# Performance work log

Hardware: AMD Instinct MI355X
Metric: run time of the kernel (lower is better)

## Reference

```python
import jax, jax.numpy as jnp
import numpy as np

D_MODEL = 768
N_HEADS = 12
D_K = D_MODEL // N_HEADS
NEG_INF = -1e9


def setup_inputs() -> dict:
    key = jax.random.key(0)
    ks = jax.random.split(key, 7)
    B, S = 4, 2048
    x = jax.random.normal(ks[0], (B, S, D_MODEL), dtype=jnp.float32)
    # causal mask, broadcastable to [B, H, S, S]
    mask = jnp.tril(jnp.ones((S, S), dtype=bool))[None, None, :, :]
    scale = 1.0 / np.sqrt(D_MODEL)
    Wq = jax.random.normal(ks[1], (D_MODEL, D_MODEL), dtype=jnp.float32) * scale
    bq = jnp.zeros((D_MODEL,), dtype=jnp.float32)
    Wk = jax.random.normal(ks[2], (D_MODEL, D_MODEL), dtype=jnp.float32) * scale
    bk = jnp.zeros((D_MODEL,), dtype=jnp.float32)
    Wv = jax.random.normal(ks[3], (D_MODEL, D_MODEL), dtype=jnp.float32) * scale
    bv = jnp.zeros((D_MODEL,), dtype=jnp.float32)
    return {"x": x, "mask": mask, "Wq": Wq, "bq": bq, "Wk": Wk, "bk": bk, "Wv": Wv, "bv": bv}


def reference(x, mask, Wq, bq, Wk, bk, Wv, bv):
    B, S, _ = x.shape
    # projections (torch Linear: y = x @ W.T + b)
    q = (x @ Wq.T + bq).reshape(B, S, N_HEADS, D_K)
    k = (x @ Wk.T + bk).reshape(B, S, N_HEADS, D_K)
    v = (x @ Wv.T + bv).reshape(B, S, N_HEADS, D_K)
    # scores: [B, H, S, S]
    scores = jnp.einsum("bqhd,bkhd->bhqk", q, k) / jnp.sqrt(jnp.float32(D_K))
    scores = jnp.where(mask, scores, NEG_INF)
    probs = jax.nn.softmax(scores, axis=-1)
    # attention: [B, H, S, D_K] -> [B, S, d_model]
    attn = jnp.einsum("bhqk,bkhd->bqhd", probs, v).reshape(B, S, D_MODEL)
    return attn
```

## Files before the change

### kernel.cpp

```cpp
#include <hip/hip_runtime.h>
#include <math.h>


#define S_LEN 2048
#define BATCH 4
#define HEADS 12
#define DM 768
#define DK 64
#define BH (BATCH*HEADS)
#define MROWS (BATCH*S_LEN)
#define QSCALE 0.1803368801111244f

typedef __attribute__((ext_vector_type(8))) short short8;
typedef __attribute__((ext_vector_type(4))) float floatx4;
typedef __attribute__((address_space(3))) unsigned char lds_byte;
typedef __attribute__((address_space(1))) const unsigned char glob_byte;

__device__ __forceinline__ unsigned short f2bf(float f) {
  union { float f; unsigned int u; } a; a.f = f;
  unsigned int u = a.u;
  return (unsigned short)((u + 0x7fffu + ((u >> 16) & 1u)) >> 16);
}
__device__ __forceinline__ unsigned short f2bf_rtz(float f) {
  union { float f; unsigned int u; } a; a.f = f;
  return (unsigned short)(a.u >> 16);
}

__global__ void cast_f32_bf16(const float* __restrict__ src,
                              unsigned short* __restrict__ dst, int n) {
  int i = (blockIdx.x * blockDim.x + threadIdx.x) * 4;
  if (i < n) {
    float4 v = *(const float4*)(src + i);
    ushort4 o;
    o.x = f2bf(v.x); o.y = f2bf(v.y); o.z = f2bf(v.z); o.w = f2bf(v.w);
    *(ushort4*)(dst + i) = o;
  }
}

__global__ void cast_w3(const float* __restrict__ w0, const float* __restrict__ w1,
                        const float* __restrict__ w2, unsigned short* __restrict__ dst,
                        int n) {
  const float* src = (blockIdx.y == 0) ? w0 : (blockIdx.y == 1) ? w1 : w2;
  int i = (blockIdx.x * blockDim.x + threadIdx.x) * 4;
  if (i < n) {
    float4 v = *(const float4*)(src + i);
    ushort4 o;
    o.x = f2bf(v.x); o.y = f2bf(v.y); o.z = f2bf(v.z); o.w = f2bf(v.w);
    *(ushort4*)(dst + (size_t)blockIdx.y * n + i) = o;
  }
}

__global__ __launch_bounds__(256) void qkv_gemm(
    const unsigned short* __restrict__ xb,
    const unsigned short* __restrict__ wb,
    const float* __restrict__ bq, const float* __restrict__ bk,
    const float* __restrict__ bv,
    unsigned short* __restrict__ qo,
    unsigned short* __restrict__ ko,
    unsigned short* __restrict__ vto) {
  __shared__ unsigned short a_lds[128 * 32];
  __shared__ unsigned short b_lds[128 * 32];
  const int mat = blockIdx.z;
  const int tid = threadIdx.x;
  const int wave = tid >> 6, lane = tid & 63, quad = lane >> 4, ln = lane & 15;
  const int wm = wave & 1, wn = wave >> 1;
  const int m_blk = blockIdx.x * 128, n_blk = blockIdx.y * 128;
  const unsigned short* w = wb + (size_t)mat * DM * DM;
  const int srow = lane >> 2, schunk = lane & 3;

  const floatx4 fz = {0.f, 0.f, 0.f, 0.f};
  floatx4 acc[4][4];
#pragma unroll
  for (int mg = 0; mg < 4; mg++)
#pragma unroll
    for (int c = 0; c < 4; c++) acc[mg][c] = fz;

  for (int k0 = 0; k0 < DM; k0 += 32) {
#pragma unroll
    for (int j = 0; j < 2; j++) {
      int row = wave * 32 + j * 16 + srow;
      __builtin_amdgcn_global_load_lds(
          (glob_byte*)(xb + (size_t)(m_blk + row) * DM + k0 + schunk * 8),
          (lds_byte*)(a_lds + (size_t)(wave * 32 + j * 16) * 32), 16, 0, 0);
      __builtin_amdgcn_global_load_lds(
          (glob_byte*)(w + (size_t)(n_blk + row) * DM + k0 + schunk * 8),
          (lds_byte*)(b_lds + (size_t)(wave * 32 + j * 16) * 32), 16, 0, 0);
    }
    __syncthreads();

    short8 af[4], bf[4];
#pragma unroll
    for (int mg = 0; mg < 4; mg++)
      af[mg] = *(const short8*)(a_lds + (wm * 64 + mg * 16 + ln) * 32 + quad * 8);
#pragma unroll
    for (int c = 0; c < 4; c++)
      bf[c] = *(const short8*)(b_lds + (wn * 64 + c * 16 + ln) * 32 + quad * 8);
#pragma unroll
    for (int mg = 0; mg < 4; mg++)
#pragma unroll
      for (int c = 0; c < 4; c++)
        acc[mg][c] = __builtin_amdgcn_mfma_f32_16x16x32_bf16(af[mg], bf[c], acc[mg][c], 0, 0, 0);
    __syncthreads();
  }

  const float* bias = (mat == 0) ? bq : (mat == 1) ? bk : bv;
  const float oscale = (mat == 0) ? QSCALE : 1.0f;
  const int m_base = m_blk + wm * 64, n_base = n_blk + wn * 64;
#pragma unroll
  for (int mg = 0; mg < 4; mg++)
#pragma unroll
    for (int c = 0; c < 4; c++) {
      int gn = n_base + c * 16 + ln;
      int hd = gn >> 6, d = gn & 63;
      float bias_v = bias[gn] * oscale;
      int gm0 = m_base + mg * 16 + quad * 4;
      int bb = gm0 >> 11, s0 = gm0 & (S_LEN - 1);
      if (mat == 2) {
        ushort4 pk;
        pk.x = f2bf(acc[mg][c][0] + bias_v);
        pk.y = f2bf(acc[mg][c][1] + bias_v);
        pk.z = f2bf(acc[mg][c][2] + bias_v);
        pk.w = f2bf(acc[mg][c][3] + bias_v);
        *(ushort4*)(vto + (((size_t)(bb * HEADS + hd)) * DK + d) * S_LEN + s0) = pk;
      } else {
        unsigned short* dst = (mat == 0 ? qo : ko) +
            (((size_t)(bb * HEADS + hd)) * S_LEN + s0) * DK + d;
#pragma unroll
        for (int r = 0; r < 4; r++)
          dst[(size_t)r * DK] = f2bf(acc[mg][c][r] * oscale + bias_v);
      }
    }
}

__global__ __launch_bounds__(128) void flash_attn(
    const unsigned short* __restrict__ q,
    const unsigned short* __restrict__ k,
    const unsigned short* __restrict__ vt,
    float* __restrict__ out) {
  __shared__ unsigned short p_lds[2][32 * 64];
  const int id = blockIdx.x;
  const int bh = id % BH;
  const int qt = (S_LEN / 64 - 1) - (id / BH);
  const int q0 = qt * 64;
  const int tid = threadIdx.x;
  const int wave = tid >> 6, lane = tid & 63, quad = lane >> 4, ln = lane & 15;
  unsigned short* pl = p_lds[wave];
  const unsigned short* qp = q  + (size_t)bh * S_LEN * DK;
  const unsigned short* kp = k  + (size_t)bh * S_LEN * DK;
  const unsigned short* vp = vt + (size_t)bh * DK * S_LEN;
  const int qr_base = q0 + wave * 32;
  const floatx4 fz = {0.f, 0.f, 0.f, 0.f};

  unsigned short* wp[4];
#pragma unroll
  for (int kg = 0; kg < 4; kg++)
    wp[kg] = pl + quad * 256 + (((((kg ^ quad) & 3) << 1) | (ln >> 3)) * 8) + (ln & 7);
  const unsigned short* rp[2];
#pragma unroll
  for (int ss = 0; ss < 2; ss++)
    rp[ss] = pl + ln * 64 + (((ss * 4 + quad) ^ (((ln >> 2) & 3) << 1)) * 8);

  const int klane = ln * DK + quad * 8;
  const int vlane = ln * S_LEN + quad * 8;

  short8 ones;
#pragma unroll
  for (int j = 0; j < 8; j++) ones[j] = (short)0x3F80;

  short8 aq[2][2];
#pragma unroll
  for (int h = 0; h < 2; h++)
#pragma unroll
    for (int ss = 0; ss < 2; ss++)
      aq[h][ss] = *(const short8*)(qp + (qr_base + h * 16 + ln) * DK + ss * 32 + quad * 8);

  floatx4 o[2][4];
  floatx4 ol[2] = {fz, fz};
#pragma unroll
  for (int h = 0; h < 2; h++) {
    o[h][0] = fz; o[h][1] = fz; o[h][2] = fz; o[h][3] = fz;
  }

  const int kend = qr_base + 32;
  for (int k0 = 0; k0 < kend; k0 += 64) {
    short8 kf[4][2];
#pragma unroll
    for (int kg = 0; kg < 4; kg++)
#pragma unroll
      for (int ss = 0; ss < 2; ss++)
        kf[kg][ss] = *(const short8*)(kp + klane + (k0 + kg * 16) * DK + ss * 32);

    floatx4 sc[2][4];
#pragma unroll
    for (int h = 0; h < 2; h++)
#pragma unroll
      for (int kg = 0; kg < 4; kg++) {
        floatx4 tt = __builtin_amdgcn_mfma_f32_16x16x32_bf16(aq[h][0], kf[kg][0], fz, 0, 0, 0);
        sc[h][kg] = __builtin_amdgcn_mfma_f32_16x16x32_bf16(aq[h][1], kf[kg][1], tt, 0, 0, 0);
      }

    short8 vf[4][2];
#pragma unroll
    for (int dg = 0; dg < 4; dg++)
#pragma unroll
      for (int ss = 0; ss < 2; ss++)
        vf[dg][ss] = *(const short8*)(vp + vlane + dg * 16 * S_LEN + k0 + ss * 32);

    const bool domask = (k0 + 63 > qr_base);
#pragma unroll
    for (int h = 0; h < 2; h++)
#pragma unroll
      for (int kg = 0; kg < 4; kg++) {
        int key = k0 + kg * 16 + ln;
#pragma unroll
        for (int r = 0; r < 4; r++) {
          float pv = exp2f(sc[h][kg][r]);
          if (domask) {
            int qr = qr_base + h * 16 + quad * 4 + r;
            pv = (key <= qr) ? pv : 0.f;
          }
          wp[kg][h * 1024 + r * 64] = f2bf_rtz(pv);
        }
      }

    short8 ap[2][2];
#pragma unroll
    for (int h = 0; h < 2; h++)
#pragma unroll
      for (int ss = 0; ss < 2; ss++)
        ap[h][ss] = *(const short8*)(rp[ss] + h * 1024);

#pragma unroll
    for (int h = 0; h < 2; h++) {
#pragma unroll
      for (int dg = 0; dg < 4; dg++) {
        o[h][dg] = __builtin_amdgcn_mfma_f32_16x16x32_bf16(ap[h][0], vf[dg][0], o[h][dg], 0, 0, 0);
        o[h][dg] = __builtin_amdgcn_mfma_f32_16x16x32_bf16(ap[h][1], vf[dg][1], o[h][dg], 0, 0, 0);
      }
      ol[h] = __builtin_amdgcn_mfma_f32_16x16x32_bf16(ap[h][0], ones, ol[h], 0, 0, 0);
      ol[h] = __builtin_amdgcn_mfma_f32_16x16x32_bf16(ap[h][1], ones, ol[h], 0, 0, 0);
    }
  }

  const int b = bh / HEADS, hd = bh % HEADS;
#pragma unroll
  for (int h = 0; h < 2; h++)
#pragma unroll
    for (int r = 0; r < 4; r++) {
      float inv = 1.f / ol[h][r];
      int qr = qr_base + h * 16 + quad * 4 + r;
      float* orow = out + ((size_t)(b * S_LEN + qr)) * DM + hd * DK;
      orow[ln]      = o[h][0][r] * inv;
      orow[16 + ln] = o[h][1][r] * inv;
      orow[32 + ln] = o[h][2][r] * inv;
      orow[48 + ln] = o[h][3][r] * inv;
    }
}

extern "C" void kernel_launch(void* const* d_in, const int* in_sizes, int n_in,
                              void* d_out, int out_size, void* d_ws, size_t ws_size,
                              hipStream_t stream) {
  const float* x  = (const float*)d_in[0];
  const float* Wq = (const float*)d_in[2];
  const float* bq = (const float*)d_in[3];
  const float* Wk = (const float*)d_in[4];
  const float* bk = (const float*)d_in[5];
  const float* Wv = (const float*)d_in[6];
  const float* bv = (const float*)d_in[7];
  float* out = (float*)d_out;

  const int NX = MROWS * DM;
  const int NW = DM * DM;
  unsigned short* xb = (unsigned short*)d_ws;
  unsigned short* wb = xb + NX;
  unsigned short* qo = wb + 3 * NW;
  unsigned short* ko = qo + (size_t)BH * S_LEN * DK;
  unsigned short* vt = ko + (size_t)BH * S_LEN * DK;

  cast_f32_bf16<<<(NX / 4 + 255) / 256, 256, 0, stream>>>(x, xb, NX);
  cast_w3<<<dim3((NW / 4 + 255) / 256, 3), 256, 0, stream>>>(Wq, Wk, Wv, wb, NW);

  qkv_gemm<<<dim3(MROWS / 128, DM / 128, 3), 256, 0, stream>>>(
      xb, wb, bq, bk, bv, qo, ko, vt);

  flash_attn<<<dim3((S_LEN / 64) * BH), 128, 0, stream>>>(qo, ko, vt, out);
}
```

Before: 254.8 us.

## Double-buffer K fragments in registers and interleave per-head-row attention work

The attention loop is unrolled by two, and the next 64-key K tile is loaded into a second register buffer while the current tile is computed, so global K loads overlap MFMA work. Score, exp, LDS write-back and PV MFMAs now run per 16-row half (h) instead of as separate phases, which shortens the live range of the score accumulators. The trade-off is more registers for the second K buffer, which could lower occupancy. The prefetch can also read K rows past the causal bound, and past the tensor end for the last head.

```diff
diff --git a/kernel.cpp b/kernel.cpp
--- a/kernel.cpp
+++ b/kernel.cpp
@@ -181,40 +181,36 @@
     o[h][0] = fz; o[h][1] = fz; o[h][2] = fz; o[h][3] = fz;
   }
 
-  const int kend = qr_base + 32;
-  for (int k0 = 0; k0 < kend; k0 += 64) {
-    short8 kf[4][2];
+  auto loadK = [&](int k0, short8 (&kf)[4][2]) {
 #pragma unroll
     for (int kg = 0; kg < 4; kg++)
 #pragma unroll
       for (int ss = 0; ss < 2; ss++)
         kf[kg][ss] = *(const short8*)(kp + klane + (k0 + kg * 16) * DK + ss * 32);
-
-    floatx4 sc[2][4];
-#pragma unroll
-    for (int h = 0; h < 2; h++)
+  };
+
+  auto body = [&](int k0, short8 (&kf)[4][2]) {
+    short8 vf[4][2];
+#pragma unroll
+    for (int dg = 0; dg < 4; dg++)
+#pragma unroll
+      for (int ss = 0; ss < 2; ss++)
+        vf[dg][ss] = *(const short8*)(vp + vlane + dg * 16 * S_LEN + k0 + ss * 32);
+    const bool domask = (k0 + 63 > qr_base);
+#pragma unroll
+    for (int h = 0; h < 2; h++) {
+      floatx4 sc[4];
 #pragma unroll
       for (int kg = 0; kg < 4; kg++) {
         floatx4 tt = __builtin_amdgcn_mfma_f32_16x16x32_bf16(aq[h][0], kf[kg][0], fz, 0, 0, 0);
-        sc[h][kg] = __builtin_amdgcn_mfma_f32_16x16x32_bf16(aq[h][1], kf[kg][1], tt, 0, 0, 0);
-      }
-
-    short8 vf[4][2];
-#pragma unroll
-    for (int dg = 0; dg < 4; dg++)
-#pragma unroll
-      for (int ss = 0; ss < 2; ss++)
-        vf[dg][ss] = *(const short8*)(vp + vlane + dg * 16 * S_LEN + k0 + ss * 32);
-
-    const bool domask = (k0 + 63 > qr_base);
-#pragma unroll
-    for (int h = 0; h < 2; h++)
+        sc[kg] = __builtin_amdgcn_mfma_f32_16x16x32_bf16(aq[h][1], kf[kg][1], tt, 0, 0, 0);
+      }
 #pragma unroll
       for (int kg = 0; kg < 4; kg++) {
         int key = k0 + kg * 16 + ln;
 #pragma unroll
         for (int r = 0; r < 4; r++) {
-          float pv = exp2f(sc[h][kg][r]);
+          float pv = exp2f(sc[kg][r]);
           if (domask) {
             int qr = qr_base + h * 16 + quad * 4 + r;
             pv = (key <= qr) ? pv : 0.f;
@@ -222,25 +218,29 @@
           wp[kg][h * 1024 + r * 64] = f2bf_rtz(pv);
         }
       }
-
-    short8 ap[2][2];
-#pragma unroll
-    for (int h = 0; h < 2; h++)
-#pragma unroll
-      for (int ss = 0; ss < 2; ss++)
-        ap[h][ss] = *(const short8*)(rp[ss] + h * 1024);
-
-#pragma unroll
-    for (int h = 0; h < 2; h++) {
+      short8 ap0 = *(const short8*)(rp[0] + h * 1024);
+      short8 ap1 = *(const short8*)(rp[1] + h * 1024);
 #pragma unroll
       for (int dg = 0; dg < 4; dg++) {
-        o[h][dg] = __builtin_amdgcn_mfma_f32_16x16x32_bf16(ap[h][0], vf[dg][0], o[h][dg], 0, 0, 0);
-        o[h][dg] = __builtin_amdgcn_mfma_f32_16x16x32_bf16(ap[h][1], vf[dg][1], o[h][dg], 0, 0, 0);
-      }
-      ol[h] = __builtin_amdgcn_mfma_f32_16x16x32_bf16(ap[h][0], ones, ol[h], 0, 0, 0);
-      ol[h] = __builtin_amdgcn_mfma_f32_16x16x32_bf16(ap[h][1], ones, ol[h], 0, 0, 0);
-    }
-  }
+        o[h][dg] = __builtin_amdgcn_mfma_f32_16x16x32_bf16(ap0, vf[dg][0], o[h][dg], 0, 0, 0);
+        o[h][dg] = __builtin_amdgcn_mfma_f32_16x16x32_bf16(ap1, vf[dg][1], o[h][dg], 0, 0, 0);
+      }
+      ol[h] = __builtin_amdgcn_mfma_f32_16x16x32_bf16(ap0, ones, ol[h], 0, 0, 0);
+      ol[h] = __builtin_amdgcn_mfma_f32_16x16x32_bf16(ap1, ones, ol[h], 0, 0, 0);
+    }
+  };
+
+  const int kend = qr_base + 32;
+  short8 kfa[4][2], kfb[4][2];
+  loadK(0, kfa);
+  int k0 = 0;
+  for (; k0 + 64 < kend; k0 += 128) {
+    loadK(k0 + 64, kfb);
+    body(k0, kfa);
+    loadK(k0 + 128, kfa);
+    body(k0 + 64, kfb);
+  }
+  if (k0 < kend) body(k0, kfa);
 
   const int b = bh / HEADS, hd = bh % HEADS;
 #pragma unroll
```

New measurement: 256.5 us. About the same (+0.7%).
